# Performance work log

Measured on AMD Instinct MI355X. Metric: run time of the kernel, lower is better.

Reference implementation:

```python
import jax, jax.numpy as jnp
import numpy as np

IN_F = 4096
OUT_F = 12288
GROUPSIZE = 128
BATCH = 8
N_GROUPS = IN_F // GROUPSIZE  # 32


def setup_inputs() -> dict:
    key = jax.random.key(0)
    k1, k2, k3, k4 = jax.random.split(key, 4)
    x = jax.random.normal(k1, (BATCH, IN_F), dtype=jnp.float32)
    # int4 codes in [0, 16)
    qweight = jax.random.randint(k2, (OUT_F, IN_F), 0, 16, dtype=jnp.int32)
    # per-group scales (positive, small) and zeros, layout [in//groupsize, out]
    scales = jax.random.uniform(k3, (N_GROUPS, OUT_F), dtype=jnp.float32) * 0.02 + 1e-3
    zeros = jax.random.normal(k4, (N_GROUPS, OUT_F), dtype=jnp.float32) * 0.1
    return {"x": x, "qweight": qweight, "scales": scales, "zeros": zeros}


def reference(x, qweight, scales, zeros):
    # Dequantize int4 weights: w = (q - 8) * scale + zero, per group of 128 along K.
    # qweight: [OUT_F, IN_F] -> [OUT_F, N_GROUPS, GROUPSIZE]
    q = qweight.reshape(OUT_F, N_GROUPS, GROUPSIZE).astype(jnp.float32)
    s = scales.T[:, :, None]  # [OUT_F, N_GROUPS, 1]
    z = zeros.T[:, :, None]   # [OUT_F, N_GROUPS, 1]
    w = ((q - 8.0) * s + z).reshape(OUT_F, IN_F)  # dequantized fp weight
    # Linear: y = x @ w.T  -> [BATCH, OUT_F]
    return jnp.einsum('bk,nk->bn', x, w)
```

## Files before the change

kernel.cpp:

```cpp
#include <hip/hip_runtime.h>

#define IN_F 4096
#define OUT_F 12288
#define BATCH 8
#define NGROUPS 32

#define ROWS_PER_WAVE 3
#define ROWS_PER_BLOCK 48
#define NBLOCKS (OUT_F / ROWS_PER_BLOCK)
#define THREADS 1024
#define CHUNK 256
#define NCHUNKS (IN_F / CHUNK)

typedef int v4i __attribute__((ext_vector_type(4)));

__global__ __launch_bounds__(THREADS, 4)
void w4a32_gemv(const float* __restrict__ x,
                const int* __restrict__ qw,
                const float* __restrict__ scales,
                const float* __restrict__ zeros,
                float* __restrict__ out)
{
    __shared__ float xs[BATCH][IN_F];
    __shared__ float szs[NGROUPS * ROWS_PER_BLOCK];
    __shared__ float szc[NGROUPS * ROWS_PER_BLOCK];

    const int tid   = threadIdx.x;
    const int wave  = tid >> 6;
    const int lane  = tid & 63;
    const int rowb  = blockIdx.x * ROWS_PER_BLOCK;
    const int wrow  = wave * ROWS_PER_WAVE;
    const int klane = lane << 2;

    const int* __restrict__ qbase = qw + (size_t)(rowb + wrow) * IN_F + klane;

#define ISSUE(B, c) do {                                                     \
    _Pragma("unroll")                                                        \
    for (int r = 0; r < ROWS_PER_WAVE; ++r)                                  \
        B[r] = *reinterpret_cast<const v4i*>(qbase + r * IN_F + (c) * CHUNK);\
    } while (0)

    v4i qA[ROWS_PER_WAVE], qB[ROWS_PER_WAVE];
    ISSUE(qA, 0);

#pragma unroll
    for (int j = 0; j < 8; ++j) {
        const int idx = tid + j * THREADS;
        const int b   = idx >> 10;
        const int kk  = (idx & 1023) << 2;
        *reinterpret_cast<float4*>(&xs[b][kk]) =
            *reinterpret_cast<const float4*>(&x[b * IN_F + kk]);
    }
#pragma unroll
    for (int j = 0; j < 2; ++j) {
        const int idx = tid + j * THREADS;
        const int g   = idx >> 6;
        const int r   = idx & 63;
        if (r < ROWS_PER_BLOCK) {
            const float s = scales[g * OUT_F + rowb + r];
            const float z = zeros [g * OUT_F + rowb + r];
            szs[g * ROWS_PER_BLOCK + r] = s;
            szc[g * ROWS_PER_BLOCK + r] = __builtin_fmaf(s, -8.f, z);
        }
    }
    __syncthreads();

    float acc[ROWS_PER_WAVE][BATCH];
#pragma unroll
    for (int r = 0; r < ROWS_PER_WAVE; ++r)
#pragma unroll
        for (int b = 0; b < BATCH; ++b) acc[r][b] = 0.f;

#define CONSUME(B, c) do {                                                   \
    const int g = 2 * (c) + (lane >> 5);                                     \
    float4 xr[BATCH];                                                        \
    _Pragma("unroll")                                                        \
    for (int b = 0; b < BATCH; ++b)                                          \
        xr[b] = *reinterpret_cast<const float4*>(&xs[b][(c) * CHUNK + klane]);\
    _Pragma("unroll")                                                        \
    for (int r = 0; r < ROWS_PER_WAVE; ++r) {                                \
        const float s  = szs[g * ROWS_PER_BLOCK + wrow + r];                 \
        const float cc = szc[g * ROWS_PER_BLOCK + wrow + r];                 \
        const float w0 = __builtin_fmaf((float)B[r][0], s, cc);              \
        const float w1 = __builtin_fmaf((float)B[r][1], s, cc);              \
        const float w2 = __builtin_fmaf((float)B[r][2], s, cc);              \
        const float w3 = __builtin_fmaf((float)B[r][3], s, cc);              \
        _Pragma("unroll")                                                    \
        for (int b = 0; b < BATCH; ++b) {                                    \
            float a = acc[r][b];                                             \
            a = __builtin_fmaf(w0, xr[b].x, a);                              \
            a = __builtin_fmaf(w1, xr[b].y, a);                              \
            a = __builtin_fmaf(w2, xr[b].z, a);                              \
            a = __builtin_fmaf(w3, xr[b].w, a);                              \
            acc[r][b] = a;                                                   \
        }                                                                    \
    } } while (0)

    for (int c = 0; c < NCHUNKS; c += 2) {
        ISSUE(qB, c + 1);
        CONSUME(qA, c);
        if (c + 2 < NCHUNKS) ISSUE(qA, c + 2);
        CONSUME(qB, c + 1);
    }
#undef ISSUE
#undef CONSUME

#pragma unroll
    for (int r = 0; r < ROWS_PER_WAVE; ++r) {
        const int n = rowb + wrow + r;
#pragma unroll
        for (int b = 0; b < BATCH; ++b) {
            float v = acc[r][b];
            v += __shfl_xor(v, 32);
            v += __shfl_xor(v, 16);
            v += __shfl_xor(v, 8);
            v += __shfl_xor(v, 4);
            v += __shfl_xor(v, 2);
            v += __shfl_xor(v, 1);
            if (lane == b) out[b * OUT_F + n] = v;
        }
    }
}

extern "C" void kernel_launch(void* const* d_in, const int* in_sizes, int n_in,
                              void* d_out, int out_size, void* d_ws, size_t ws_size,
                              hipStream_t stream) {
    const float* x      = (const float*)d_in[0];
    const int*   qw     = (const int*)d_in[1];
    const float* scales = (const float*)d_in[2];
    const float* zeros  = (const float*)d_in[3];
    float* out = (float*)d_out;

    w4a32_gemv<<<NBLOCKS, THREADS, 0, stream>>>(x, qw, scales, zeros, out);
}
```

Measured before the change: 43.04 us.

## Batch weight loads into four-chunk superblocks and reorder FMA loop

Replaces the two-buffer ping-pong prefetch with superblocks of four chunks per row. The next superblock's loads are issued after the last chunk's weights are dequantized, so more global loads are in flight per wave, and it also swaps the loop order so each x vector is loaded once and used across rows. This is meant to hide memory latency in a bandwidth-bound GEMV, at the cost of more registers and lower occupancy. It also leaves a gap with no loads in flight while the first three chunks of each superblock are consumed.

```diff
diff --git a/kernel.cpp b/kernel.cpp
--- a/kernel.cpp
+++ b/kernel.cpp
@@ -11,6 +11,8 @@
 #define THREADS 1024
 #define CHUNK 256
 #define NCHUNKS (IN_F / CHUNK)
+#define SB 4
+#define NSB (NCHUNKS / SB)
 
 typedef int v4i __attribute__((ext_vector_type(4)));
 
@@ -34,14 +36,17 @@
 
     const int* __restrict__ qbase = qw + (size_t)(rowb + wrow) * IN_F + klane;
 
-#define ISSUE(B, c) do {                                                     \
+#define ISSUE_SB(Q, s) do {                                                  \
     _Pragma("unroll")                                                        \
     for (int r = 0; r < ROWS_PER_WAVE; ++r)                                  \
-        B[r] = *reinterpret_cast<const v4i*>(qbase + r * IN_F + (c) * CHUNK);\
+        _Pragma("unroll")                                                    \
+        for (int c = 0; c < SB; ++c)                                         \
+            Q[r][c] = *reinterpret_cast<const v4i*>(                         \
+                qbase + r * IN_F + ((s) * SB + c) * CHUNK);                  \
     } while (0)
 
-    v4i qA[ROWS_PER_WAVE], qB[ROWS_PER_WAVE];
-    ISSUE(qA, 0);
+    v4i q[ROWS_PER_WAVE][SB];
+    ISSUE_SB(q, 0);
 
 #pragma unroll
     for (int j = 0; j < 8; ++j) {
@@ -71,39 +76,42 @@
 #pragma unroll
         for (int b = 0; b < BATCH; ++b) acc[r][b] = 0.f;
 
-#define CONSUME(B, c) do {                                                   \
-    const int g = 2 * (c) + (lane >> 5);                                     \
-    float4 xr[BATCH];                                                        \
-    _Pragma("unroll")                                                        \
-    for (int b = 0; b < BATCH; ++b)                                          \
-        xr[b] = *reinterpret_cast<const float4*>(&xs[b][(c) * CHUNK + klane]);\
-    _Pragma("unroll")                                                        \
-    for (int r = 0; r < ROWS_PER_WAVE; ++r) {                                \
-        const float s  = szs[g * ROWS_PER_BLOCK + wrow + r];                 \
-        const float cc = szc[g * ROWS_PER_BLOCK + wrow + r];                 \
-        const float w0 = __builtin_fmaf((float)B[r][0], s, cc);              \
-        const float w1 = __builtin_fmaf((float)B[r][1], s, cc);              \
-        const float w2 = __builtin_fmaf((float)B[r][2], s, cc);              \
-        const float w3 = __builtin_fmaf((float)B[r][3], s, cc);              \
-        _Pragma("unroll")                                                    \
-        for (int b = 0; b < BATCH; ++b) {                                    \
-            float a = acc[r][b];                                             \
-            a = __builtin_fmaf(w0, xr[b].x, a);                              \
-            a = __builtin_fmaf(w1, xr[b].y, a);                              \
-            a = __builtin_fmaf(w2, xr[b].z, a);                              \
-            a = __builtin_fmaf(w3, xr[b].w, a);                              \
-            acc[r][b] = a;                                                   \
-        }                                                                    \
-    } } while (0)
+    for (int s = 0; s < NSB; ++s) {
+#pragma unroll
+        for (int c = 0; c < SB; ++c) {
+            const int cc = s * SB + c;
+            const int g  = 2 * cc + (lane >> 5);
 
-    for (int c = 0; c < NCHUNKS; c += 2) {
-        ISSUE(qB, c + 1);
-        CONSUME(qA, c);
-        if (c + 2 < NCHUNKS) ISSUE(qA, c + 2);
-        CONSUME(qB, c + 1);
+            float w[ROWS_PER_WAVE][4];
+#pragma unroll
+            for (int r = 0; r < ROWS_PER_WAVE; ++r) {
+                const float sc = szs[g * ROWS_PER_BLOCK + wrow + r];
+                const float cz = szc[g * ROWS_PER_BLOCK + wrow + r];
+                w[r][0] = __builtin_fmaf((float)q[r][c][0], sc, cz);
+                w[r][1] = __builtin_fmaf((float)q[r][c][1], sc, cz);
+                w[r][2] = __builtin_fmaf((float)q[r][c][2], sc, cz);
+                w[r][3] = __builtin_fmaf((float)q[r][c][3], sc, cz);
+            }
+
+            if (c == SB - 1 && s + 1 < NSB) ISSUE_SB(q, s + 1);
+
+#pragma unroll
+            for (int b = 0; b < BATCH; ++b) {
+                const float4 xb =
+                    *reinterpret_cast<const float4*>(&xs[b][cc * CHUNK + klane]);
+#pragma unroll
+                for (int r = 0; r < ROWS_PER_WAVE; ++r) {
+                    float a = acc[r][b];
+                    a = __builtin_fmaf(w[r][0], xb.x, a);
+                    a = __builtin_fmaf(w[r][1], xb.y, a);
+                    a = __builtin_fmaf(w[r][2], xb.z, a);
+                    a = __builtin_fmaf(w[r][3], xb.w, a);
+                    acc[r][b] = a;
+                }
+            }
+        }
     }
-#undef ISSUE
-#undef CONSUME
+#undef ISSUE_SB
 
 #pragma unroll
     for (int r = 0; r < ROWS_PER_WAVE; ++r) {
```

Result: slower. 138.1 us (+220.8%).
